# Kernel tuning notes

Measured on AMD Instinct MI355X. Metric: run time of the kernel, lower is better.

The kernel has to match this reference:

```python
import jax, jax.numpy as jnp
import numpy as np


def setup_inputs() -> dict:
    key = jax.random.key(0)
    k1, k2, k3 = jax.random.split(key, 3)
    B, C, T = 8, 256, 4096
    H, K = 512, 4
    x = jax.random.normal(k1, (B, C, T), dtype=jnp.float32)
    W = jax.random.normal(k2, (H, C * K), dtype=jnp.float32) * 0.02
    b = jax.random.normal(k3, (H,), dtype=jnp.float32) * 0.02
    return {"x": x, "W": W, "b": b}


def reference(x, W, b):
    # Causal conv1d equivalent of the per-step Linear loop (stride=1).
    # Original flattens window as view(B, C*K): channel-major -> W[h, c*K + k].
    B, C, T = x.shape
    H = W.shape[0]
    K = W.shape[1] // C
    kernel = W.reshape(H, C, K)  # OIH layout
    out = jax.lax.conv_general_dilated(
        x, kernel,
        window_strides=(1,),
        padding=[(K - 1, 0)],  # left-pad only => causal
        dimension_numbers=("NCH", "OIH", "NCH"),
    )
    return out + b[None, :, None]  # (B, H, T)
```

## Files before the change

kernel.cpp:

```cpp
#include <hip/hip_runtime.h>
#include <hip/hip_bf16.h>


#define Bb 8
#define Cc 256
#define Tt 4096
#define Hh 512
#define Kk 4

typedef __attribute__((ext_vector_type(8))) short bf16x8;
typedef __attribute__((ext_vector_type(4))) float f32x4;

#define WS_XT_OFF   0
#define WS_WT_OFF   16777216
#define WS_ZERO_OFF 17825792
#define WS_NEEDED   17826816ULL

__device__ __forceinline__ void gload16(const void* g, void* l) {
    __builtin_amdgcn_global_load_lds(
        (const __attribute__((address_space(1))) void*)g,
        (__attribute__((address_space(3))) void*)l, 16, 0, 0);
}

__global__ __launch_bounds__(256) void prep_kernel(const float* __restrict__ x,
                                                   const float* __restrict__ W,
                                                   __hip_bfloat16* __restrict__ xT,
                                                   __hip_bfloat16* __restrict__ Wt,
                                                   float* __restrict__ zeros) {
    __shared__ __hip_bfloat16 tile[64][72];
    const int bid = blockIdx.x;
    if (bid < 2048) {
        const int t0 = (bid & 63) * 64, c0 = ((bid >> 6) & 3) * 64, b = bid >> 8;
        const int lt = threadIdx.x & 63, lw = threadIdx.x >> 6;
#pragma unroll
        for (int i = 0; i < 16; ++i) {
            int cc = lw + i * 4;
            tile[cc][lt] = __float2bfloat16(x[((size_t)(b * Cc + c0 + cc)) * Tt + t0 + lt]);
        }
        __syncthreads();
#pragma unroll
        for (int i = 0; i < 2; ++i) {
            int tt = (threadIdx.x >> 3) + i * 32;
            int c8 = threadIdx.x & 7;
            short tmp[8];
#pragma unroll
            for (int j = 0; j < 8; ++j) {
                __hip_bfloat16 v = tile[c8 * 8 + j][tt];
                tmp[j] = *reinterpret_cast<short*>(&v);
            }
            *reinterpret_cast<bf16x8*>(&xT[((size_t)(b * Tt + t0 + tt)) * Cc + c0 + c8 * 8]) =
                *reinterpret_cast<bf16x8*>(tmp);
        }
    } else {
        int n = (bid - 2048) * 256 + threadIdx.x;
        int c = n & 255;
        int h = (n >> 8) & 511;
        int k = n >> 17;
        Wt[n] = __float2bfloat16(W[h * (Cc * Kk) + c * Kk + k]);
        if (bid == 2048) zeros[threadIdx.x] = 0.f;
    }
}

#define A_STRIDE 32768
#define B_BASE   98304
#define B_STRIDE 17408
#define LDS_TOTAL 133120

#define BAR __builtin_amdgcn_s_barrier()
#define LGKM0 do { asm volatile("s_waitcnt lgkmcnt(0)" ::: "memory"); \
                   __builtin_amdgcn_sched_barrier(0); } while (0)

__global__ __launch_bounds__(512, 1) void conv_mfma_kernel(
    const __hip_bfloat16* __restrict__ xT,
    const __hip_bfloat16* __restrict__ Wt,
    const float* __restrict__ bias,
    const float* __restrict__ zeros,
    float* __restrict__ out)
{
    __shared__ __align__(1024) char smem[LDS_TOTAL];
    const int tid = threadIdx.x, lane = tid & 63, wave = tid >> 6;
    const int wr = wave >> 2, wc = wave & 3;
    const int l15 = lane & 15, lg = lane >> 4;

    const int nf = (blockIdx.x & 7) * 32 + (blockIdx.x >> 3);
    const int t0 = (nf & 15) * 256;
    const int h0 = ((nf >> 4) & 1) * 256;
    const int b  = nf >> 5;

    const char* Wt_c = (const char*)Wt;
    const char* xT_c = (const char*)xT;
    const char* zz   = (const char*)zeros;

    const char* asrc[4]; int adst[4];
#pragma unroll
    for (int i = 0; i < 4; ++i) {
        int s = tid + i * 512;
        int kk = s >> 10, row = (s >> 2) & 255, sl = s & 3;
        int colch = (sl ^ ((row >> 1) & 3)) * 8;
        asrc[i] = Wt_c + (((size_t)(kk * Hh + h0 + row)) * Cc + colch) * 2;
        adst[i] = s * 16;
    }
    const char* bsrc[2]; int bdst[2];
#pragma unroll
    for (int i = 0; i < 2; ++i) {
        int s = tid + i * 512;
        int row = s >> 2, sl = s & 3;
        int colch = (sl ^ ((row >> 1) & 3)) * 8;
        int tg = t0 - 3 + row;
        bsrc[i] = (tg >= 0 && tg < Tt)
                ? xT_c + (((size_t)b * Tt + tg) * Cc + colch) * 2 : zz;
        bdst[i] = s * 16;
    }
    const char* btsrc; {
        int row = 256 + (lane >> 2), sl = lane & 3;
        int colch = (sl ^ ((row >> 1) & 3)) * 8;
        int tg = t0 - 3 + row;
        btsrc = (row <= 258 && tg < Tt)
              ? xT_c + (((size_t)b * Tt + tg) * Cc + colch) * 2 : zz;
    }

    const int aoffb = (wr * 128 + l15) * 64 + ((lg ^ ((l15 >> 1) & 3)) << 4);
    int bofftab[4];
#pragma unroll
    for (int k = 0; k < 4; ++k)
        bofftab[k] = (wc * 64 + l15 + k) * 64 + ((lg ^ (((l15 + k) >> 1) & 3)) << 4);
    const int boff0 = bofftab[0], boff1 = bofftab[1];
    const int boff2 = bofftab[2], boff3 = bofftab[3];

    f32x4 acc[8][4] = {};

#pragma unroll
    for (int i = 0; i < 4; ++i) gload16(asrc[i], smem + adst[i]);
#pragma unroll
    for (int i = 0; i < 2; ++i) gload16(bsrc[i], smem + B_BASE + bdst[i]);
    gload16(btsrc, smem + B_BASE + 16384);
#pragma unroll
    for (int i = 0; i < 4; ++i) gload16(asrc[i] + 524288, smem + A_STRIDE + adst[i]);
    asm volatile("s_waitcnt vmcnt(4)" ::: "memory");
    BAR;

#pragma unroll
    for (int s = 0; s < 16; ++s) {
        const char* Ab  = smem + (s % 3) * A_STRIDE;
        const char* Bbf = smem + B_BASE + ((s >> 1) & 1) * B_STRIDE;
        char* And = smem + ((s + 2) % 3) * A_STRIDE;
        char* Bnd = smem + B_BASE + (((s >> 1) + 1) & 1) * B_STRIDE;
        const bool doA = (s + 2) <= 15;
        const bool doB = ((s & 1) == 0) && ((s >> 1) + 1 <= 7);
        const long aadv = (long)((s + 2) & 1) * 524288 + (long)((s + 2) >> 1) * 64;
        const int  badv = ((s >> 1) + 1) * 64;
        const int  bo0 = (s & 1) ? boff2 : boff0;
        const int  bo1 = (s & 1) ? boff3 : boff1;

        bf16x8 a_[4], b_[4];
#pragma unroll
        for (int fm = 0; fm < 4; ++fm) a_[fm] = *(const bf16x8*)(Ab + aoffb + fm * 1024);
#pragma unroll
        for (int ft = 0; ft < 4; ++ft) b_[ft] = *(const bf16x8*)(Bbf + bo0 + ft * 1024);
        if (doA) { gload16(asrc[0] + aadv, And + adst[0]); gload16(asrc[1] + aadv, And + adst[1]); }
        BAR; LGKM0;
        __builtin_amdgcn_s_setprio(1);
#pragma unroll
        for (int fm = 0; fm < 4; ++fm)
#pragma unroll
            for (int ft = 0; ft < 4; ++ft)
                acc[fm][ft] = __builtin_amdgcn_mfma_f32_16x16x32_bf16(a_[fm], b_[ft], acc[fm][ft], 0, 0, 0);
        __builtin_amdgcn_s_setprio(0);
        BAR;
#pragma unroll
        for (int fm = 0; fm < 4; ++fm) a_[fm] = *(const bf16x8*)(Ab + aoffb + (fm + 4) * 1024);
        if (doA) { gload16(asrc[2] + aadv, And + adst[2]); gload16(asrc[3] + aadv, And + adst[3]); }
        BAR; LGKM0;
        __builtin_amdgcn_s_setprio(1);
#pragma unroll
        for (int fm = 0; fm < 4; ++fm)
#pragma unroll
            for (int ft = 0; ft < 4; ++ft)
                acc[fm + 4][ft] = __builtin_amdgcn_mfma_f32_16x16x32_bf16(a_[fm], b_[ft], acc[fm + 4][ft], 0, 0, 0);
        __builtin_amdgcn_s_setprio(0);
        BAR;
#pragma unroll
        for (int fm = 0; fm < 4; ++fm) a_[fm] = *(const bf16x8*)(Ab + 16384 + aoffb + fm * 1024);
#pragma unroll
        for (int ft = 0; ft < 4; ++ft) b_[ft] = *(const bf16x8*)(Bbf + bo1 + ft * 1024);
        if (doB) { gload16(bsrc[0] + badv, Bnd + bdst[0]); gload16(bsrc[1] + badv, Bnd + bdst[1]); }
        BAR; LGKM0;
        __builtin_amdgcn_s_setprio(1);
#pragma unroll
        for (int fm = 0; fm < 4; ++fm)
#pragma unroll
            for (int ft = 0; ft < 4; ++ft)
                acc[fm][ft] = __builtin_amdgcn_mfma_f32_16x16x32_bf16(a_[fm], b_[ft], acc[fm][ft], 0, 0, 0);
        __builtin_amdgcn_s_setprio(0);
        BAR;
#pragma unroll
        for (int fm = 0; fm < 4; ++fm) a_[fm] = *(const bf16x8*)(Ab + 16384 + aoffb + (fm + 4) * 1024);
        if (doB) gload16(btsrc + badv, Bnd + 16384);
        BAR; LGKM0;
        __builtin_amdgcn_s_setprio(1);
#pragma unroll
        for (int fm = 0; fm < 4; ++fm)
#pragma unroll
            for (int ft = 0; ft < 4; ++ft)
                acc[fm + 4][ft] = __builtin_amdgcn_mfma_f32_16x16x32_bf16(a_[fm], b_[ft], acc[fm + 4][ft], 0, 0, 0);
        __builtin_amdgcn_s_setprio(0);
        if (s < 14) {
            if ((s & 1) == 0) asm volatile("s_waitcnt vmcnt(7)" ::: "memory");
            else              asm volatile("s_waitcnt vmcnt(4)" ::: "memory");
        } else if (s == 14)   asm volatile("s_waitcnt vmcnt(0)" ::: "memory");
        BAR;
    }

#pragma unroll
    for (int fm = 0; fm < 8; ++fm) {
        int hb = h0 + wr * 128 + fm * 16 + lg * 4;
        float4 bs = *(const float4*)&bias[hb];
        const float* bsp = (const float*)&bs;
#pragma unroll
        for (int q = 0; q < 4; ++q)
#pragma unroll
            for (int ft = 0; ft < 4; ++ft) {
                int t = t0 + wc * 64 + ft * 16 + l15;
                out[((size_t)(b * Hh + hb + q)) * Tt + t] = acc[fm][ft][q] + bsp[q];
            }
    }
}

#define TT 256
#define HT 8
#define CT 4
__global__ __launch_bounds__(256) void conv1d_f32_kernel(
    const float* __restrict__ x, const float* __restrict__ W,
    const float* __restrict__ bias, float* __restrict__ out)
{
    const int tid = threadIdx.x;
    const int t0 = blockIdx.x * TT;
    const int h0 = blockIdx.y * HT;
    const int b  = blockIdx.z;
    __shared__ float xs[CT][TT + Kk];
    float acc[HT];
#pragma unroll
    for (int h = 0; h < HT; ++h) acc[h] = 0.f;
    const float* xb = x + (size_t)b * Cc * Tt;
    for (int c0 = 0; c0 < Cc; c0 += CT) {
        __syncthreads();
#pragma unroll
        for (int cc = 0; cc < CT; ++cc)
            for (int j = tid; j < TT + Kk - 1; j += 256) {
                int idx = t0 - (Kk - 1) + j;
                xs[cc][j] = (idx >= 0) ? xb[(size_t)(c0 + cc) * Tt + idx] : 0.f;
            }
        __syncthreads();
#pragma unroll
        for (int cc = 0; cc < CT; ++cc) {
            float xv[Kk];
#pragma unroll
            for (int k = 0; k < Kk; ++k) xv[k] = xs[cc][tid + k];
#pragma unroll
            for (int h = 0; h < HT; ++h) {
                const float* wp = W + (size_t)(h0 + h) * (Cc * Kk) + (size_t)(c0 + cc) * Kk;
#pragma unroll
                for (int k = 0; k < Kk; ++k) acc[h] += wp[k] * xv[k];
            }
        }
    }
#pragma unroll
    for (int h = 0; h < HT; ++h)
        out[((size_t)b * Hh + (h0 + h)) * Tt + t0 + tid] = acc[h] + bias[h0 + h];
}

extern "C" void kernel_launch(void* const* d_in, const int* in_sizes, int n_in,
                              void* d_out, int out_size, void* d_ws, size_t ws_size,
                              hipStream_t stream) {
    const float* x    = (const float*)d_in[0];
    const float* W    = (const float*)d_in[1];
    const float* bias = (const float*)d_in[2];
    float* out        = (float*)d_out;

    if (ws_size >= WS_NEEDED) {
        __hip_bfloat16* xT = (__hip_bfloat16*)((char*)d_ws + WS_XT_OFF);
        __hip_bfloat16* Wt = (__hip_bfloat16*)((char*)d_ws + WS_WT_OFF);
        float* zeros       = (float*)((char*)d_ws + WS_ZERO_OFF);

        prep_kernel<<<dim3(4096), dim3(256), 0, stream>>>(x, W, xT, Wt, zeros);
        conv_mfma_kernel<<<dim3(256), dim3(512), 0, stream>>>(xT, Wt, bias, zeros, out);
    } else {
        conv1d_f32_kernel<<<dim3(Tt / TT, Hh / HT, Bb), dim3(256), 0, stream>>>(x, W, bias, out);
    }
}
```

Baseline: 50.67 us.

## Halve MFMA conv tile to 256x128 with 4 waves, two blocks per CU

Changes the conv GEMM tiling from 512-thread blocks with a 256x256 output tile to 256-thread blocks with a 256x128 tile. The grid grows from 256 to 512 blocks, and launch bounds now allow two blocks per CU. The pipeline is rebuilt as 32 K-steps of 64 channels, with triple-buffered A and double-buffered B tiles and smaller LDS buffers. The goal is better occupancy, better CU load balance and latency hiding between co-resident blocks, at the cost of reloading the weight tiles twice as often.

After: 51.14 us. About the same (+0.9%).

```diff
diff --git a/kernel.cpp b/kernel.cpp
--- a/kernel.cpp
+++ b/kernel.cpp
@@ -61,16 +61,16 @@
     }
 }
 
-#define A_STRIDE 32768
-#define B_BASE   98304
-#define B_STRIDE 17408
-#define LDS_TOTAL 133120
+#define A_BUF   16384
+#define B_BUF   12288
+#define B_BASE  49152
+#define LDS_TOTAL 73728
 
 #define BAR __builtin_amdgcn_s_barrier()
 #define LGKM0 do { asm volatile("s_waitcnt lgkmcnt(0)" ::: "memory"); \
                    __builtin_amdgcn_sched_barrier(0); } while (0)
 
-__global__ __launch_bounds__(512, 1) void conv_mfma_kernel(
+__global__ __launch_bounds__(256, 2) void conv_mfma_kernel(
     const __hip_bfloat16* __restrict__ xT,
     const __hip_bfloat16* __restrict__ Wt,
     const float* __restrict__ bias,
@@ -79,85 +79,77 @@
 {
     __shared__ __align__(1024) char smem[LDS_TOTAL];
     const int tid = threadIdx.x, lane = tid & 63, wave = tid >> 6;
-    const int wr = wave >> 2, wc = wave & 3;
+    const int wr = wave >> 1, wc = wave & 1;
     const int l15 = lane & 15, lg = lane >> 4;
 
-    const int nf = (blockIdx.x & 7) * 32 + (blockIdx.x >> 3);
-    const int t0 = (nf & 15) * 256;
-    const int h0 = ((nf >> 4) & 1) * 256;
-    const int b  = nf >> 5;
+    const int flat = blockIdx.x + 32 * blockIdx.y + 64 * blockIdx.z;
+    const int swz  = (flat & 7) * 64 + (flat >> 3);
+    const int t0 = (swz & 31) * 128;
+    const int h0 = ((swz >> 5) & 1) * 256;
+    const int b  = swz >> 6;
 
     const char* Wt_c = (const char*)Wt;
     const char* xT_c = (const char*)xT;
     const char* zz   = (const char*)zeros;
 
-    const char* asrc[4]; int adst[4];
+    const char* abase[4]; int adst_[4];
 #pragma unroll
     for (int i = 0; i < 4; ++i) {
-        int s = tid + i * 512;
-        int kk = s >> 10, row = (s >> 2) & 255, sl = s & 3;
+        int s = tid + i * 256;
+        int row = s >> 2, sl = s & 3;
         int colch = (sl ^ ((row >> 1) & 3)) * 8;
-        asrc[i] = Wt_c + (((size_t)(kk * Hh + h0 + row)) * Cc + colch) * 2;
-        adst[i] = s * 16;
-    }
-    const char* bsrc[2]; int bdst[2];
-#pragma unroll
-    for (int i = 0; i < 2; ++i) {
-        int s = tid + i * 512;
+        abase[i] = Wt_c + (((size_t)(h0 + row)) * Cc + colch) * 2;
+        adst_[i] = s * 16;
+    }
+    const char* bbase[3]; int bdst_[3];
+#pragma unroll
+    for (int i = 0; i < 3; ++i) {
+        int s = tid + i * 256;
         int row = s >> 2, sl = s & 3;
         int colch = (sl ^ ((row >> 1) & 3)) * 8;
         int tg = t0 - 3 + row;
-        bsrc[i] = (tg >= 0 && tg < Tt)
-                ? xT_c + (((size_t)b * Tt + tg) * Cc + colch) * 2 : zz;
-        bdst[i] = s * 16;
-    }
-    const char* btsrc; {
-        int row = 256 + (lane >> 2), sl = lane & 3;
-        int colch = (sl ^ ((row >> 1) & 3)) * 8;
-        int tg = t0 - 3 + row;
-        btsrc = (row <= 258 && tg < Tt)
-              ? xT_c + (((size_t)b * Tt + tg) * Cc + colch) * 2 : zz;
-    }
-
-    const int aoffb = (wr * 128 + l15) * 64 + ((lg ^ ((l15 >> 1) & 3)) << 4);
-    int bofftab[4];
+        bool valid = (row <= 130) && (tg >= 0);
+        bbase[i] = valid ? xT_c + (((size_t)b * Tt + tg) * Cc + colch) * 2
+                         : zz + (s & 31) * 16;
+        bdst_[i] = s * 16;
+    }
+
+    const int aoff0 = (wr * 128 + l15) * 64 + ((lg ^ ((l15 >> 1) & 3)) << 4);
+    int btab[4];
 #pragma unroll
     for (int k = 0; k < 4; ++k)
-        bofftab[k] = (wc * 64 + l15 + k) * 64 + ((lg ^ (((l15 + k) >> 1) & 3)) << 4);
-    const int boff0 = bofftab[0], boff1 = bofftab[1];
-    const int boff2 = bofftab[2], boff3 = bofftab[3];
-
-    f32x4 acc[8][4] = {};
-
-#pragma unroll
-    for (int i = 0; i < 4; ++i) gload16(asrc[i], smem + adst[i]);
-#pragma unroll
-    for (int i = 0; i < 2; ++i) gload16(bsrc[i], smem + B_BASE + bdst[i]);
-    gload16(btsrc, smem + B_BASE + 16384);
-#pragma unroll
-    for (int i = 0; i < 4; ++i) gload16(asrc[i] + 524288, smem + A_STRIDE + adst[i]);
+        btab[k] = (wc * 64 + l15 + k) * 64 + ((lg ^ (((l15 + k) >> 1) & 3)) << 4);
+
+    char *A0 = smem, *A1 = smem + A_BUF, *A2 = smem + 2 * A_BUF;
+    char *B0 = smem + B_BASE, *B1 = smem + B_BASE + B_BUF;
+
+#pragma unroll
+    for (int i = 0; i < 4; ++i) gload16(abase[i], A0 + adst_[i]);
+#pragma unroll
+    for (int i = 0; i < 3; ++i) gload16(bbase[i], B0 + bdst_[i]);
+#pragma unroll
+    for (int i = 0; i < 4; ++i) gload16(abase[i] + 262144, A1 + adst_[i]);
     asm volatile("s_waitcnt vmcnt(4)" ::: "memory");
     BAR;
 
-#pragma unroll
-    for (int s = 0; s < 16; ++s) {
-        const char* Ab  = smem + (s % 3) * A_STRIDE;
-        const char* Bbf = smem + B_BASE + ((s >> 1) & 1) * B_STRIDE;
-        char* And = smem + ((s + 2) % 3) * A_STRIDE;
-        char* Bnd = smem + B_BASE + (((s >> 1) + 1) & 1) * B_STRIDE;
-        const bool doA = (s + 2) <= 15;
-        const bool doB = ((s & 1) == 0) && ((s >> 1) + 1 <= 7);
-        const long aadv = (long)((s + 2) & 1) * 524288 + (long)((s + 2) >> 1) * 64;
-        const int  badv = ((s >> 1) + 1) * 64;
-        const int  bo0 = (s & 1) ? boff2 : boff0;
-        const int  bo1 = (s & 1) ? boff3 : boff1;
+    f32x4 acc[8][4] = {};
+
+#pragma unroll 4
+    for (int s = 0; s < 32; ++s) {
+        const int kap = s & 3;
+        const int bo  = (kap == 0) ? btab[0] : (kap == 1) ? btab[1]
+                      : (kap == 2) ? btab[2] : btab[3];
 
         bf16x8 a_[4], b_[4];
 #pragma unroll
-        for (int fm = 0; fm < 4; ++fm) a_[fm] = *(const bf16x8*)(Ab + aoffb + fm * 1024);
-#pragma unroll
-        for (int ft = 0; ft < 4; ++ft) b_[ft] = *(const bf16x8*)(Bbf + bo0 + ft * 1024);
-        if (doA) { gload16(asrc[0] + aadv, And + adst[0]); gload16(asrc[1] + aadv, And + adst[1]); }
+        for (int fm = 0; fm < 4; ++fm) a_[fm] = *(const bf16x8*)(A0 + aoff0 + fm * 1024);
+#pragma unroll
+        for (int ft = 0; ft < 4; ++ft) b_[ft] = *(const bf16x8*)(B0 + bo + ft * 1024);
+        if (s < 30) {
+            const long au = (long)((s + 2) & 3) * 262144 + (long)((s + 2) >> 2) * 64;
+#pragma unroll
+            for (int i = 0; i < 4; ++i) gload16(abase[i] + au, A2 + adst_[i]);
+        }
         BAR; LGKM0;
         __builtin_amdgcn_s_setprio(1);
 #pragma unroll
@@ -168,8 +160,12 @@
         __builtin_amdgcn_s_setprio(0);
         BAR;
 #pragma unroll
-        for (int fm = 0; fm < 4; ++fm) a_[fm] = *(const bf16x8*)(Ab + aoffb + (fm + 4) * 1024);
-        if (doA) { gload16(asrc[2] + aadv, And + adst[2]); gload16(asrc[3] + aadv, And + adst[3]); }
+        for (int fm = 0; fm < 4; ++fm) a_[fm] = *(const bf16x8*)(A0 + aoff0 + (fm + 4) * 1024);
+        if (kap == 0 && s < 28) {
+            const long bu = (long)((s >> 2) + 1) * 64;
+#pragma unroll
+            for (int i = 0; i < 3; ++i) gload16(bbase[i] + bu, B1 + bdst_[i]);
+        }
         BAR; LGKM0;
         __builtin_amdgcn_s_setprio(1);
 #pragma unroll
@@ -178,37 +174,13 @@
             for (int ft = 0; ft < 4; ++ft)
                 acc[fm + 4][ft] = __builtin_amdgcn_mfma_f32_16x16x32_bf16(a_[fm], b_[ft], acc[fm + 4][ft], 0, 0, 0);
         __builtin_amdgcn_s_setprio(0);
+        if (s < 30) {
+            if (kap == 0 && s < 28) asm volatile("s_waitcnt vmcnt(7)" ::: "memory");
+            else                    asm volatile("s_waitcnt vmcnt(4)" ::: "memory");
+        } else if (s == 30)         asm volatile("s_waitcnt vmcnt(0)" ::: "memory");
         BAR;
-#pragma unroll
-        for (int fm = 0; fm < 4; ++fm) a_[fm] = *(const bf16x8*)(Ab + 16384 + aoffb + fm * 1024);
-#pragma unroll
-        for (int ft = 0; ft < 4; ++ft) b_[ft] = *(const bf16x8*)(Bbf + bo1 + ft * 1024);
-        if (doB) { gload16(bsrc[0] + badv, Bnd + bdst[0]); gload16(bsrc[1] + badv, Bnd + bdst[1]); }
-        BAR; LGKM0;
-        __builtin_amdgcn_s_setprio(1);
-#pragma unroll
-        for (int fm = 0; fm < 4; ++fm)
-#pragma unroll
-            for (int ft = 0; ft < 4; ++ft)
-                acc[fm][ft] = __builtin_amdgcn_mfma_f32_16x16x32_bf16(a_[fm], b_[ft], acc[fm][ft], 0, 0, 0);
-        __builtin_amdgcn_s_setprio(0);
-        BAR;
-#pragma unroll
-        for (int fm = 0; fm < 4; ++fm) a_[fm] = *(const bf16x8*)(Ab + 16384 + aoffb + (fm + 4) * 1024);
-        if (doB) gload16(btsrc + badv, Bnd + 16384);
-        BAR; LGKM0;
-        __builtin_amdgcn_s_setprio(1);
-#pragma unroll
-        for (int fm = 0; fm < 4; ++fm)
-#pragma unroll
-            for (int ft = 0; ft < 4; ++ft)
-                acc[fm + 4][ft] = __builtin_amdgcn_mfma_f32_16x16x32_bf16(a_[fm], b_[ft], acc[fm + 4][ft], 0, 0, 0);
-        __builtin_amdgcn_s_setprio(0);
-        if (s < 14) {
-            if ((s & 1) == 0) asm volatile("s_waitcnt vmcnt(7)" ::: "memory");
-            else              asm volatile("s_waitcnt vmcnt(4)" ::: "memory");
-        } else if (s == 14)   asm volatile("s_waitcnt vmcnt(0)" ::: "memory");
-        BAR;
+        char* tp = A0; A0 = A1; A1 = A2; A2 = tp;
+        if (kap == 3) { char* up = B0; B0 = B1; B1 = up; }
     }
 
 #pragma unroll
@@ -283,7 +255,7 @@
         float* zeros       = (float*)((char*)d_ws + WS_ZERO_OFF);
 
         prep_kernel<<<dim3(4096), dim3(256), 0, stream>>>(x, W, xT, Wt, zeros);
-        conv_mfma_kernel<<<dim3(256), dim3(512), 0, stream>>>(xT, Wt, bias, zeros, out);
+        conv_mfma_kernel<<<dim3(32, 2, 8), dim3(256), 0, stream>>>(xT, Wt, bias, zeros, out);
     } else {
         conv1d_f32_kernel<<<dim3(Tt / TT, Hh / HT, Bb), dim3(256), 0, stream>>>(x, W, bias, out);
     }
```

## Pre-tile weights in LDS slot order and prefetch MFMA fragments a phase ahead

Applied to the files above, without the earlier changes.

The prep kernel now writes the bf16 weights in the exact swizzled order in which each conv block loads its LDS stage, so A-tile global loads become contiguous offsets from one base pointer instead of per-thread strided addresses. The main loop is re-pipelined so the LDS fragments for the next MFMA phase are read before the current phase's barrier, and the lgkmcnt waits are partial rather than full drains. This lets LDS reads overlap with MFMA work and cuts address arithmetic. The cost is more live fragment registers per thread and a more delicate wait/barrier ordering.

Measured after the change: 49.53 us, median of 2. -2.2%, faster.

```diff
diff --git a/kernel.cpp b/kernel.cpp
--- a/kernel.cpp
+++ b/kernel.cpp
@@ -25,7 +25,7 @@
 __global__ __launch_bounds__(256) void prep_kernel(const float* __restrict__ x,
                                                    const float* __restrict__ W,
                                                    __hip_bfloat16* __restrict__ xT,
-                                                   __hip_bfloat16* __restrict__ Wt,
+                                                   __hip_bfloat16* __restrict__ Wt2,
                                                    float* __restrict__ zeros) {
     __shared__ __hip_bfloat16 tile[64][72];
     const int bid = blockIdx.x;
@@ -52,11 +52,16 @@
                 *reinterpret_cast<bf16x8*>(tmp);
         }
     } else {
-        int n = (bid - 2048) * 256 + threadIdx.x;
-        int c = n & 255;
-        int h = (n >> 8) & 511;
-        int k = n >> 17;
-        Wt[n] = __float2bfloat16(W[h * (Cc * Kk) + c * Kk + k]);
+        int n2 = (bid - 2048) * 256 + threadIdx.x;
+        int e   = n2 & 7;
+        int s   = (n2 >> 3) & 2047;
+        int st  = (n2 >> 14) & 15;
+        int h0t = n2 >> 18;
+        int row = (s >> 2) & 255, sl = s & 3, kk = s >> 10;
+        int c = (st >> 1) * 32 + ((sl ^ ((row >> 1) & 3)) << 3) + e;
+        int k = (st & 1) * 2 + kk;
+        int h = h0t * 256 + row;
+        Wt2[n2] = __float2bfloat16(W[h * (Cc * Kk) + c * Kk + k]);
         if (bid == 2048) zeros[threadIdx.x] = 0.f;
     }
 }
@@ -67,12 +72,12 @@
 #define LDS_TOTAL 133120
 
 #define BAR __builtin_amdgcn_s_barrier()
-#define LGKM0 do { asm volatile("s_waitcnt lgkmcnt(0)" ::: "memory"); \
-                   __builtin_amdgcn_sched_barrier(0); } while (0)
+#define LGKM(n) do { asm volatile("s_waitcnt lgkmcnt(" #n ")" ::: "memory"); \
+                     __builtin_amdgcn_sched_barrier(0); } while (0)
 
 __global__ __launch_bounds__(512, 1) void conv_mfma_kernel(
     const __hip_bfloat16* __restrict__ xT,
-    const __hip_bfloat16* __restrict__ Wt,
+    const __hip_bfloat16* __restrict__ Wt2,
     const float* __restrict__ bias,
     const float* __restrict__ zeros,
     float* __restrict__ out)
@@ -87,19 +92,14 @@
     const int h0 = ((nf >> 4) & 1) * 256;
     const int b  = nf >> 5;
 
-    const char* Wt_c = (const char*)Wt;
+    const char* aW   = (const char*)Wt2 + (h0 >> 8) * 524288;
     const char* xT_c = (const char*)xT;
     const char* zz   = (const char*)zeros;
 
-    const char* asrc[4]; int adst[4];
-#pragma unroll
-    for (int i = 0; i < 4; ++i) {
-        int s = tid + i * 512;
-        int kk = s >> 10, row = (s >> 2) & 255, sl = s & 3;
-        int colch = (sl ^ ((row >> 1) & 3)) * 8;
-        asrc[i] = Wt_c + (((size_t)(kk * Hh + h0 + row)) * Cc + colch) * 2;
-        adst[i] = s * 16;
-    }
+    int aslot[4];
+#pragma unroll
+    for (int i = 0; i < 4; ++i) aslot[i] = (tid + i * 512) * 16;
+
     const char* bsrc[2]; int bdst[2];
 #pragma unroll
     for (int i = 0; i < 2; ++i) {
@@ -130,12 +130,12 @@
     f32x4 acc[8][4] = {};
 
 #pragma unroll
-    for (int i = 0; i < 4; ++i) gload16(asrc[i], smem + adst[i]);
+    for (int i = 0; i < 4; ++i) gload16(aW + aslot[i], smem + aslot[i]);
 #pragma unroll
     for (int i = 0; i < 2; ++i) gload16(bsrc[i], smem + B_BASE + bdst[i]);
     gload16(btsrc, smem + B_BASE + 16384);
 #pragma unroll
-    for (int i = 0; i < 4; ++i) gload16(asrc[i] + 524288, smem + A_STRIDE + adst[i]);
+    for (int i = 0; i < 4; ++i) gload16(aW + 32768 + aslot[i], smem + A_STRIDE + aslot[i]);
     asm volatile("s_waitcnt vmcnt(4)" ::: "memory");
     BAR;
 
@@ -147,67 +147,74 @@
         char* Bnd = smem + B_BASE + (((s >> 1) + 1) & 1) * B_STRIDE;
         const bool doA = (s + 2) <= 15;
         const bool doB = ((s & 1) == 0) && ((s >> 1) + 1 <= 7);
-        const long aadv = (long)((s + 2) & 1) * 524288 + (long)((s + 2) >> 1) * 64;
-        const int  badv = ((s >> 1) + 1) * 64;
+        const long aoffg = (long)(s + 2) * 32768;
+        const int  badv  = ((s >> 1) + 1) * 64;
         const int  bo0 = (s & 1) ? boff2 : boff0;
         const int  bo1 = (s & 1) ? boff3 : boff1;
 
-        bf16x8 a_[4], b_[4];
-#pragma unroll
-        for (int fm = 0; fm < 4; ++fm) a_[fm] = *(const bf16x8*)(Ab + aoffb + fm * 1024);
-#pragma unroll
-        for (int ft = 0; ft < 4; ++ft) b_[ft] = *(const bf16x8*)(Bbf + bo0 + ft * 1024);
-        if (doA) { gload16(asrc[0] + aadv, And + adst[0]); gload16(asrc[1] + aadv, And + adst[1]); }
-        BAR; LGKM0;
-        __builtin_amdgcn_s_setprio(1);
-#pragma unroll
-        for (int fm = 0; fm < 4; ++fm)
-#pragma unroll
-            for (int ft = 0; ft < 4; ++ft)
-                acc[fm][ft] = __builtin_amdgcn_mfma_f32_16x16x32_bf16(a_[fm], b_[ft], acc[fm][ft], 0, 0, 0);
-        __builtin_amdgcn_s_setprio(0);
-        BAR;
-#pragma unroll
-        for (int fm = 0; fm < 4; ++fm) a_[fm] = *(const bf16x8*)(Ab + aoffb + (fm + 4) * 1024);
-        if (doA) { gload16(asrc[2] + aadv, And + adst[2]); gload16(asrc[3] + aadv, And + adst[3]); }
-        BAR; LGKM0;
-        __builtin_amdgcn_s_setprio(1);
-#pragma unroll
-        for (int fm = 0; fm < 4; ++fm)
-#pragma unroll
-            for (int ft = 0; ft < 4; ++ft)
-                acc[fm + 4][ft] = __builtin_amdgcn_mfma_f32_16x16x32_bf16(a_[fm], b_[ft], acc[fm + 4][ft], 0, 0, 0);
-        __builtin_amdgcn_s_setprio(0);
-        BAR;
-#pragma unroll
-        for (int fm = 0; fm < 4; ++fm) a_[fm] = *(const bf16x8*)(Ab + 16384 + aoffb + fm * 1024);
-#pragma unroll
-        for (int ft = 0; ft < 4; ++ft) b_[ft] = *(const bf16x8*)(Bbf + bo1 + ft * 1024);
-        if (doB) { gload16(bsrc[0] + badv, Bnd + bdst[0]); gload16(bsrc[1] + badv, Bnd + bdst[1]); }
-        BAR; LGKM0;
-        __builtin_amdgcn_s_setprio(1);
-#pragma unroll
-        for (int fm = 0; fm < 4; ++fm)
-#pragma unroll
-            for (int ft = 0; ft < 4; ++ft)
-                acc[fm][ft] = __builtin_amdgcn_mfma_f32_16x16x32_bf16(a_[fm], b_[ft], acc[fm][ft], 0, 0, 0);
-        __builtin_amdgcn_s_setprio(0);
-        BAR;
-#pragma unroll
-        for (int fm = 0; fm < 4; ++fm) a_[fm] = *(const bf16x8*)(Ab + 16384 + aoffb + (fm + 4) * 1024);
+        bf16x8 fA0[4], fB0[4], fA1[4], fA2[4], fB2[4], fA3[4];
+
+#pragma unroll
+        for (int fm = 0; fm < 4; ++fm) fA0[fm] = *(const bf16x8*)(Ab + aoffb + fm * 1024);
+#pragma unroll
+        for (int ft = 0; ft < 4; ++ft) fB0[ft] = *(const bf16x8*)(Bbf + bo0 + ft * 1024);
+#pragma unroll
+        for (int fm = 0; fm < 4; ++fm) fA1[fm] = *(const bf16x8*)(Ab + aoffb + (fm + 4) * 1024);
+        if (doA) { gload16(aW + aoffg + aslot[0], And + aslot[0]);
+                   gload16(aW + aoffg + aslot[1], And + aslot[1]); }
+        BAR; LGKM(4);
+        __builtin_amdgcn_s_setprio(1);
+#pragma unroll
+        for (int fm = 0; fm < 4; ++fm)
+#pragma unroll
+            for (int ft = 0; ft < 4; ++ft)
+                acc[fm][ft] = __builtin_amdgcn_mfma_f32_16x16x32_bf16(fA0[fm], fB0[ft], acc[fm][ft], 0, 0, 0);
+        __builtin_amdgcn_s_setprio(0);
+        BAR;
+
+#pragma unroll
+        for (int fm = 0; fm < 4; ++fm) fA2[fm] = *(const bf16x8*)(Ab + 16384 + aoffb + fm * 1024);
+#pragma unroll
+        for (int ft = 0; ft < 4; ++ft) fB2[ft] = *(const bf16x8*)(Bbf + bo1 + ft * 1024);
+        if (doA) { gload16(aW + aoffg + aslot[2], And + aslot[2]);
+                   gload16(aW + aoffg + aslot[3], And + aslot[3]); }
+        BAR; LGKM(8);
+        __builtin_amdgcn_s_setprio(1);
+#pragma unroll
+        for (int fm = 0; fm < 4; ++fm)
+#pragma unroll
+            for (int ft = 0; ft < 4; ++ft)
+                acc[fm + 4][ft] = __builtin_amdgcn_mfma_f32_16x16x32_bf16(fA1[fm], fB0[ft], acc[fm + 4][ft], 0, 0, 0);
+        __builtin_amdgcn_s_setprio(0);
+        BAR;
+
+#pragma unroll
+        for (int fm = 0; fm < 4; ++fm) fA3[fm] = *(const bf16x8*)(Ab + 16384 + aoffb + (fm + 4) * 1024);
+        if (doB) { gload16(bsrc[0] + badv, Bnd + bdst[0]);
+                   gload16(bsrc[1] + badv, Bnd + bdst[1]); }
+        BAR; LGKM(4);
+        __builtin_amdgcn_s_setprio(1);
+#pragma unroll
+        for (int fm = 0; fm < 4; ++fm)
+#pragma unroll
+            for (int ft = 0; ft < 4; ++ft)
+                acc[fm][ft] = __builtin_amdgcn_mfma_f32_16x16x32_bf16(fA2[fm], fB2[ft], acc[fm][ft], 0, 0, 0);
+        __builtin_amdgcn_s_setprio(0);
+        BAR;
+
         if (doB) gload16(btsrc + badv, Bnd + 16384);
-        BAR; LGKM0;
-        __builtin_amdgcn_s_setprio(1);
-#pragma unroll
-        for (int fm = 0; fm < 4; ++fm)
-#pragma unroll
-            for (int ft = 0; ft < 4; ++ft)
-                acc[fm + 4][ft] = __builtin_amdgcn_mfma_f32_16x16x32_bf16(a_[fm], b_[ft], acc[fm + 4][ft], 0, 0, 0);
-        __builtin_amdgcn_s_setprio(0);
         if (s < 14) {
             if ((s & 1) == 0) asm volatile("s_waitcnt vmcnt(7)" ::: "memory");
             else              asm volatile("s_waitcnt vmcnt(4)" ::: "memory");
         } else if (s == 14)   asm volatile("s_waitcnt vmcnt(0)" ::: "memory");
+        BAR; LGKM(0);
+        __builtin_amdgcn_s_setprio(1);
+#pragma unroll
+        for (int fm = 0; fm < 4; ++fm)
+#pragma unroll
+            for (int ft = 0; ft < 4; ++ft)
+                acc[fm + 4][ft] = __builtin_amdgcn_mfma_f32_16x16x32_bf16(fA3[fm], fB2[ft], acc[fm + 4][ft], 0, 0, 0);
+        __builtin_amdgcn_s_setprio(0);
         BAR;
     }
 
@@ -278,12 +285,12 @@
     float* out        = (float*)d_out;
 
     if (ws_size >= WS_NEEDED) {
-        __hip_bfloat16* xT = (__hip_bfloat16*)((char*)d_ws + WS_XT_OFF);
-        __hip_bfloat16* Wt = (__hip_bfloat16*)((char*)d_ws + WS_WT_OFF);
-        float* zeros       = (float*)((char*)d_ws + WS_ZERO_OFF);
-
-        prep_kernel<<<dim3(4096), dim3(256), 0, stream>>>(x, W, xT, Wt, zeros);
-        conv_mfma_kernel<<<dim3(256), dim3(512), 0, stream>>>(xT, Wt, bias, zeros, out);
+        __hip_bfloat16* xT  = (__hip_bfloat16*)((char*)d_ws + WS_XT_OFF);
+        __hip_bfloat16* Wt2 = (__hip_bfloat16*)((char*)d_ws + WS_WT_OFF);
+        float* zeros        = (float*)((char*)d_ws + WS_ZERO_OFF);
+
+        prep_kernel<<<dim3(4096), dim3(256), 0, stream>>>(x, W, xT, Wt2, zeros);
+        conv_mfma_kernel<<<dim3(256), dim3(512), 0, stream>>>(xT, Wt2, bias, zeros, out);
     } else {
         conv1d_f32_kernel<<<dim3(Tt / TT, Hh / HT, Bb), dim3(256), 0, stream>>>(x, W, bias, out);
     }
```
